# Kernel optimization log

Measured on AMD Instinct MI355X. Metric: run time of the kernel, lower is better.

## Reference

```python
import jax, jax.numpy as jnp
import numpy as np

ALPHA = 0.2  # LeakyReLU negative slope
EPS = 1e-8


def setup_inputs() -> dict:
    key = jax.random.key(0)
    k1, k2, k3, k4, k5 = jax.random.split(key, 5)
    N, D = 8192, 64  # square bipartite graph (required by the module's broadcasting)
    return {
        "user_embeddings": jax.random.normal(k1, (N, D), dtype=jnp.float32),
        "item_embeddings": jax.random.normal(k2, (N, D), dtype=jnp.float32),
        "adjacency_matrix": jax.random.uniform(k3, (N, N), dtype=jnp.float32),
        "W1": jax.random.normal(k4, (D, D), dtype=jnp.float32),
        "W2": jax.random.normal(k5, (D, D), dtype=jnp.float32),
    }


def _propagate(src, tgt, adj_st, W1, W2):
    """Fused NGCF message passing.

    Naive math: msg[a, b, :] = (src @ W1)[b, :] + (src[a] * tgt[b]) @ W2
                agg[a, :]    = sum_b adj_st[a, b] * msg[a, b, :]
    The sum over b distributes, so we never build the [N, N, D] tensor:
      agg = adj_st @ (src @ W1) + (src * (adj_st @ tgt)) @ W2
    """
    agg = adj_st @ (src @ W1) + (src * (adj_st @ tgt)) @ W2
    return jax.nn.leaky_relu(agg + tgt, negative_slope=ALPHA)


def reference(user_embeddings, item_embeddings, adjacency_matrix, W1, W2):
    # symmetric (sqrt of row-degree * col-degree) normalization
    row_sum = adjacency_matrix.sum(axis=1, keepdims=True)  # [N_u, 1]
    col_sum = adjacency_matrix.sum(axis=0, keepdims=True)  # [1, N_i]
    A = adjacency_matrix / (jnp.sqrt(row_sum * col_sum) + EPS)

    # item -> user messages use A^T; user -> item messages use A
    updated_user = _propagate(item_embeddings, user_embeddings, A.T, W1, W2)
    updated_item = _propagate(user_embeddings, item_embeddings, A, W1, W2)
    return (updated_user, updated_item)
```

## Files before the change

### kernel.cpp

```cpp
#include <hip/hip_runtime.h>
#include <hip/hip_bf16.h>


#define LRELU_ALPHA 0.2f
constexpr int N = 8192;
constexpr int KSPLIT = 8;
constexpr int KC = N / KSPLIT;

typedef __attribute__((ext_vector_type(4))) float f32x4;
typedef __attribute__((ext_vector_type(8))) __bf16 bf16x8;

__device__ __forceinline__ unsigned short f2bf(float x) {
    unsigned u = __builtin_bit_cast(unsigned, x);
    u += 0x7fffu + ((u >> 16) & 1u);
    return (unsigned short)(u >> 16);
}
__device__ __forceinline__ f32x4 mfma16(uint4 a, uint4 b, f32x4 c) {
    return __builtin_amdgcn_mfma_f32_16x16x32_bf16(
        __builtin_bit_cast(bf16x8, a), __builtin_bit_cast(bf16x8, b), c, 0, 0, 0);
}
__device__ __forceinline__ void stage16(const void* g, void* l) {
    __builtin_amdgcn_global_load_lds(
        (const __attribute__((address_space(1))) unsigned int*)g,
        (__attribute__((address_space(3))) unsigned int*)l, 16, 0, 0);
}

__global__ __launch_bounds__(256) void pass1_kernel(
    const float* __restrict__ adj,
    float* __restrict__ rs, float* __restrict__ cs,
    unsigned short* __restrict__ adjbf, unsigned short* __restrict__ adjT) {
    __shared__ unsigned short tile[128 * 128];
    __shared__ float rowsumL[128];
    __shared__ float4 colpart4[8][32];
    const int tid = threadIdx.x;
    const int g32 = tid >> 5, l32 = tid & 31;
    const int r0 = blockIdx.y * 128, c0 = blockIdx.x * 128;

    float4 colacc = make_float4(0.f, 0.f, 0.f, 0.f);
#pragma unroll 4
    for (int s = 0; s < 16; ++s) {
        const int i = s * 8 + g32;
        float4 v = *reinterpret_cast<const float4*>(adj + (size_t)(r0 + i) * N + c0 + l32 * 4);
        colacc.x += v.x; colacc.y += v.y; colacc.z += v.z; colacc.w += v.w;
        ushort4 b;
        b.x = f2bf(v.x); b.y = f2bf(v.y); b.z = f2bf(v.z); b.w = f2bf(v.w);
        *reinterpret_cast<ushort4*>(adjbf + (size_t)(r0 + i) * N + c0 + l32 * 4) = b;
        const int csw = l32 ^ (i & 31);
        *reinterpret_cast<ushort4*>(&tile[i * 128 + csw * 4]) = b;
        float rp = (v.x + v.y) + (v.z + v.w);
#pragma unroll
        for (int off = 16; off > 0; off >>= 1) rp += __shfl_down(rp, off, 32);
        if (l32 == 0) rowsumL[i] = rp;
    }
    colpart4[g32][l32] = colacc;
    __syncthreads();

    if (tid < 128) {
        atomicAdd(rs + r0 + tid, rowsumL[tid]);
        const float* cp = (const float*)colpart4;
        float s = 0.f;
#pragma unroll
        for (int w = 0; w < 8; ++w) s += cp[w * 128 + tid];
        atomicAdd(cs + c0 + tid, s);
    }

    const int i_loc = tid & 127;
    const int jhalf = tid >> 7;
#pragma unroll 8
    for (int jj = 0; jj < 64; ++jj) {
        const int j = jhalf * 64 + jj;
        unsigned short v = tile[i_loc * 128 + (((j >> 2) ^ (i_loc & 31)) * 4) + (j & 3)];
        adjT[(size_t)(c0 + j) * N + r0 + i_loc] = v;
    }
}

__global__ __launch_bounds__(256) void prep_kernel(
    const float* __restrict__ user, const float* __restrict__ item,
    const float* __restrict__ W1, const float* __restrict__ rs, const float* __restrict__ cs,
    unsigned short* __restrict__ Bti, unsigned short* __restrict__ Btu) {
    __shared__ float W1s[64][65];
    __shared__ float ru[64][65];
    __shared__ float ri[64][65];
    __shared__ unsigned short tile[128][66];
    const int tid = threadIdx.x;
    const int j0 = blockIdx.x * 64;
    for (int t = tid; t < 64 * 64; t += 256) {
        W1s[t >> 6][t & 63] = W1[t];
        ru[t >> 6][t & 63] = user[(size_t)j0 * 64 + t];
        ri[t >> 6][t & 63] = item[(size_t)j0 * 64 + t];
    }
    __syncthreads();
    for (int pass = 0; pass < 2; ++pass) {
        for (int it = 0; it < 32; ++it) {
            int idx = tid + 256 * it;
            int d = idx & 127, jl = idx >> 7;
            float scale = (pass == 0) ? rsqrtf(cs[j0 + jl]) : rsqrtf(rs[j0 + jl]);
            float v;
            if (d < 64) {
                const float(*src)[65] = (pass == 0) ? ru : ri;
                float acc = 0.f;
#pragma unroll
                for (int k = 0; k < 64; ++k) acc += src[jl][k] * W1s[k][d];
                v = acc;
            } else {
                const float(*src)[65] = (pass == 0) ? ri : ru;
                v = src[jl][d - 64];
            }
            tile[d][jl] = f2bf(v * scale);
        }
        __syncthreads();
        unsigned short* Bt = (pass == 0) ? Bti : Btu;
        for (int t = tid; t < 128 * 64; t += 256) {
            int d = t >> 6, jl = t & 63;
            Bt[(size_t)d * N + j0 + jl] = tile[d][jl];
        }
        __syncthreads();
    }
}

__global__ __launch_bounds__(256, 3) void gemm_kernel(
    const unsigned short* __restrict__ A0, const unsigned short* __restrict__ A1,
    const unsigned short* __restrict__ B0, const unsigned short* __restrict__ B1,
    float* __restrict__ P0, float* __restrict__ P1) {
    __shared__ unsigned short As[128 * 64];
    __shared__ unsigned short Bs[128 * 64];
    const unsigned short* __restrict__ A = blockIdx.z ? A1 : A0;
    const unsigned short* __restrict__ Bt = blockIdx.z ? B1 : B0;
    float* __restrict__ P = blockIdx.z ? P1 : P0;

    const int lane = threadIdx.x & 63, wave = threadIdx.x >> 6;
    const int q = lane >> 4, lm = lane & 15;
    const int wr = wave >> 1, wc = wave & 1;
    const int m0 = blockIdx.x * 128;
    const int kbase = blockIdx.y * KC;

    const int sr = wave * 32 + (lane >> 3);
    const int sc = lane & 7;

    f32x4 acc[4][4];
#pragma unroll
    for (int mt = 0; mt < 4; ++mt)
#pragma unroll
        for (int nt = 0; nt < 4; ++nt) acc[mt][nt] = (f32x4){0.f, 0.f, 0.f, 0.f};

    for (int step = 0; step < KC / 64; ++step) {
        const int k0 = kbase + step * 64;
#pragma unroll
        for (int t = 0; t < 4; ++t) {
            const int r = sr + t * 8;
            const int koff = (sc ^ (r & 7)) * 8;
            stage16(A + (size_t)(m0 + r) * N + k0 + koff, &As[(wave * 32 + t * 8) * 64]);
            stage16(Bt + (size_t)r * N + k0 + koff, &Bs[(wave * 32 + t * 8) * 64]);
        }
        __syncthreads();
#pragma unroll
        for (int kk = 0; kk < 2; ++kk) {
            uint4 af[4], bf[4];
#pragma unroll
            for (int mt = 0; mt < 4; ++mt) {
                const int ml = wr * 64 + mt * 16 + lm;
                af[mt] = *reinterpret_cast<const uint4*>(
                    &As[ml * 64 + (((kk * 4 + q) ^ (ml & 7)) * 8)]);
            }
#pragma unroll
            for (int nt = 0; nt < 4; ++nt) {
                const int nl = wc * 64 + nt * 16 + lm;
                bf[nt] = *reinterpret_cast<const uint4*>(
                    &Bs[nl * 64 + (((kk * 4 + q) ^ (nl & 7)) * 8)]);
            }
#pragma unroll
            for (int mt = 0; mt < 4; ++mt)
#pragma unroll
                for (int nt = 0; nt < 4; ++nt)
                    acc[mt][nt] = mfma16(af[mt], bf[nt], acc[mt][nt]);
        }
        __syncthreads();
    }

#pragma unroll
    for (int mt = 0; mt < 4; ++mt)
#pragma unroll
        for (int nt = 0; nt < 4; ++nt)
#pragma unroll
            for (int r = 0; r < 4; ++r) {
                const int row = m0 + wr * 64 + mt * 16 + q * 4 + r;
                const int col = wc * 64 + nt * 16 + lm;
                atomicAdd(&P[(size_t)row * 128 + col], acc[mt][nt][r]);
            }
}

__global__ __launch_bounds__(256) void epilogue_kernel(
    const float* __restrict__ user, const float* __restrict__ item,
    const float* __restrict__ W2, const float* __restrict__ rs, const float* __restrict__ cs,
    const float* __restrict__ Pi, const float* __restrict__ Pu,
    float* __restrict__ out) {
    __shared__ float W2s[64][65];
    __shared__ float gi[4][64];
    __shared__ float gu[4][64];
    const int tid = threadIdx.x;
    for (int t = tid; t < 64 * 64; t += 256) W2s[t >> 6][t & 63] = W2[t];
    const int r4 = tid >> 6, d = tid & 63;
    for (int p = 0; p < 4; ++p) {
        const int row = blockIdx.x * 16 + p * 4 + r4;
        const float invr = rsqrtf(rs[row]);
        const float invc = rsqrtf(cs[row]);
        const float u_rd = user[(size_t)row * 64 + d];
        const float i_rd = item[(size_t)row * 64 + d];
        __syncthreads();
        gi[r4][d] = u_rd * invr * Pi[(size_t)row * 128 + 64 + d];
        gu[r4][d] = i_rd * invc * Pu[(size_t)row * 128 + 64 + d];
        __syncthreads();
        float vi = invr * Pi[(size_t)row * 128 + d] + i_rd;
        float vu = invc * Pu[(size_t)row * 128 + d] + u_rd;
#pragma unroll
        for (int e = 0; e < 64; ++e) {
            vi += gi[r4][e] * W2s[e][d];
            vu += gu[r4][e] * W2s[e][d];
        }
        vi = vi > 0.f ? vi : LRELU_ALPHA * vi;
        vu = vu > 0.f ? vu : LRELU_ALPHA * vu;
        out[(size_t)row * 64 + d] = vu;
        out[(size_t)N * 64 + (size_t)row * 64 + d] = vi;
    }
}

extern "C" void kernel_launch(void* const* d_in, const int* in_sizes, int n_in,
                              void* d_out, int out_size, void* d_ws, size_t ws_size,
                              hipStream_t stream) {
    const float* user = (const float*)d_in[0];
    const float* item = (const float*)d_in[1];
    const float* adj  = (const float*)d_in[2];
    const float* W1   = (const float*)d_in[3];
    const float* W2   = (const float*)d_in[4];
    float* out = (float*)d_out;

    char* w = (char*)d_ws;
    float* Pi = (float*)w;  w += (size_t)N * 128 * 4;
    float* Pu = (float*)w;  w += (size_t)N * 128 * 4;
    float* rs = (float*)w;  w += (size_t)N * 4;
    float* cs = (float*)w;  w += (size_t)N * 4;
    unsigned short* Bti = (unsigned short*)w;  w += (size_t)N * 128 * 2;
    unsigned short* Btu = (unsigned short*)w;  w += (size_t)N * 128 * 2;
    unsigned short* adjbf = (unsigned short*)w;  w += (size_t)N * N * 2;
    unsigned short* adjT  = (unsigned short*)w;

    (void)hipMemsetAsync(Pi, 0, ((size_t)2 * N * 128 + 2 * N) * 4, stream);

    pass1_kernel<<<dim3(N / 128, N / 128), 256, 0, stream>>>(adj, rs, cs, adjbf, adjT);
    prep_kernel<<<N / 64, 256, 0, stream>>>(user, item, W1, rs, cs, Bti, Btu);
    gemm_kernel<<<dim3(N / 128, KSPLIT, 2), 256, 0, stream>>>(adjbf, adjT, Bti, Btu, Pi, Pu);
    epilogue_kernel<<<N / 16, 256, 0, stream>>>(user, item, W2, rs, cs, Pi, Pu, out);
}
```

Before: 558.9 us.

## Drop materialized transposed adjacency; transpose tiles in LDS inside a dedicated GEMM

Pass1 no longer writes a transposed bf16 copy of the adjacency matrix, which saves a 128 MB write and the matching read. A new gemmT kernel reads the row-major bf16 adjacency with plain vector loads and transposes each tile into LDS with an XOR swizzle before the MFMAs. The single batched GEMM launch becomes two launches. The transposed path does scalar 2-byte LDS stores and has no async staging for A, so its inner loop may be slower.

```diff
diff --git a/kernel.cpp b/kernel.cpp
--- a/kernel.cpp
+++ b/kernel.cpp
@@ -28,8 +28,7 @@
 __global__ __launch_bounds__(256) void pass1_kernel(
     const float* __restrict__ adj,
     float* __restrict__ rs, float* __restrict__ cs,
-    unsigned short* __restrict__ adjbf, unsigned short* __restrict__ adjT) {
-    __shared__ unsigned short tile[128 * 128];
+    unsigned short* __restrict__ adjbf) {
     __shared__ float rowsumL[128];
     __shared__ float4 colpart4[8][32];
     const int tid = threadIdx.x;
@@ -45,8 +44,6 @@
         ushort4 b;
         b.x = f2bf(v.x); b.y = f2bf(v.y); b.z = f2bf(v.z); b.w = f2bf(v.w);
         *reinterpret_cast<ushort4*>(adjbf + (size_t)(r0 + i) * N + c0 + l32 * 4) = b;
-        const int csw = l32 ^ (i & 31);
-        *reinterpret_cast<ushort4*>(&tile[i * 128 + csw * 4]) = b;
         float rp = (v.x + v.y) + (v.z + v.w);
 #pragma unroll
         for (int off = 16; off > 0; off >>= 1) rp += __shfl_down(rp, off, 32);
@@ -62,15 +59,6 @@
 #pragma unroll
         for (int w = 0; w < 8; ++w) s += cp[w * 128 + tid];
         atomicAdd(cs + c0 + tid, s);
-    }
-
-    const int i_loc = tid & 127;
-    const int jhalf = tid >> 7;
-#pragma unroll 8
-    for (int jj = 0; jj < 64; ++jj) {
-        const int j = jhalf * 64 + jj;
-        unsigned short v = tile[i_loc * 128 + (((j >> 2) ^ (i_loc & 31)) * 4) + (j & 3)];
-        adjT[(size_t)(c0 + j) * N + r0 + i_loc] = v;
     }
 }
 
@@ -118,15 +106,11 @@
     }
 }
 
-__global__ __launch_bounds__(256, 3) void gemm_kernel(
-    const unsigned short* __restrict__ A0, const unsigned short* __restrict__ A1,
-    const unsigned short* __restrict__ B0, const unsigned short* __restrict__ B1,
-    float* __restrict__ P0, float* __restrict__ P1) {
+__global__ __launch_bounds__(256, 3) void gemmN_kernel(
+    const unsigned short* __restrict__ A, const unsigned short* __restrict__ Bt,
+    float* __restrict__ P) {
     __shared__ unsigned short As[128 * 64];
     __shared__ unsigned short Bs[128 * 64];
-    const unsigned short* __restrict__ A = blockIdx.z ? A1 : A0;
-    const unsigned short* __restrict__ Bt = blockIdx.z ? B1 : B0;
-    float* __restrict__ P = blockIdx.z ? P1 : P0;
 
     const int lane = threadIdx.x & 63, wave = threadIdx.x >> 6;
     const int q = lane >> 4, lm = lane & 15;
@@ -184,6 +168,88 @@
 #pragma unroll
             for (int r = 0; r < 4; ++r) {
                 const int row = m0 + wr * 64 + mt * 16 + q * 4 + r;
+                const int col = wc * 64 + nt * 16 + lm;
+                atomicAdd(&P[(size_t)row * 128 + col], acc[mt][nt][r]);
+            }
+}
+
+__global__ __launch_bounds__(256, 3) void gemmT_kernel(
+    const unsigned short* __restrict__ A, const unsigned short* __restrict__ Bt,
+    float* __restrict__ P) {
+    __shared__ unsigned short Ts[128 * 64];
+    __shared__ unsigned short Bs[128 * 64];
+
+    const int lane = threadIdx.x & 63, wave = threadIdx.x >> 6;
+    const int q = lane >> 4, lm = lane & 15;
+    const int wr = wave >> 1, wc = wave & 1;
+    const int j0 = blockIdx.x * 128;
+    const int kbase = blockIdx.y * KC;
+
+    const int sr = wave * 32 + (lane >> 3);
+    const int sc = lane & 7;
+
+    f32x4 acc[4][4];
+#pragma unroll
+    for (int mt = 0; mt < 4; ++mt)
+#pragma unroll
+        for (int nt = 0; nt < 4; ++nt) acc[mt][nt] = (f32x4){0.f, 0.f, 0.f, 0.f};
+
+    for (int step = 0; step < KC / 64; ++step) {
+        const int ibase = kbase + step * 64;
+        uint4 g[4];
+#pragma unroll
+        for (int p = 0; p < 4; ++p) {
+            const int jc = wave + p * 4;
+            g[p] = *reinterpret_cast<const uint4*>(
+                A + (size_t)(ibase + lane) * N + j0 + jc * 8);
+        }
+        __syncthreads();
+#pragma unroll
+        for (int t = 0; t < 4; ++t) {
+            const int r = sr + t * 8;
+            const int koff = (sc ^ (r & 7)) * 8;
+            stage16(Bt + (size_t)r * N + ibase + koff, &Bs[(wave * 32 + t * 8) * 64]);
+        }
+#pragma unroll
+        for (int p = 0; p < 4; ++p) {
+            const int jl = (wave + p * 4) * 8;
+            const unsigned short* e = reinterpret_cast<const unsigned short*>(&g[p]);
+#pragma unroll
+            for (int k = 0; k < 8; ++k) {
+                Ts[(jl + k) * 64 + (lane ^ (k * 8))] = e[k];
+            }
+        }
+        __syncthreads();
+#pragma unroll
+        for (int kk = 0; kk < 2; ++kk) {
+            uint4 af[4], bf[4];
+#pragma unroll
+            for (int mt = 0; mt < 4; ++mt) {
+                const int ml = wr * 64 + mt * 16 + lm;
+                af[mt] = *reinterpret_cast<const uint4*>(
+                    &Ts[ml * 64 + ((kk * 32 + q * 8) ^ ((ml & 7) * 8))]);
+            }
+#pragma unroll
+            for (int nt = 0; nt < 4; ++nt) {
+                const int nl = wc * 64 + nt * 16 + lm;
+                bf[nt] = *reinterpret_cast<const uint4*>(
+                    &Bs[nl * 64 + (((kk * 4 + q) ^ (nl & 7)) * 8)]);
+            }
+#pragma unroll
+            for (int mt = 0; mt < 4; ++mt)
+#pragma unroll
+                for (int nt = 0; nt < 4; ++nt)
+                    acc[mt][nt] = mfma16(af[mt], bf[nt], acc[mt][nt]);
+        }
+    }
+
+#pragma unroll
+    for (int mt = 0; mt < 4; ++mt)
+#pragma unroll
+        for (int nt = 0; nt < 4; ++nt)
+#pragma unroll
+            for (int r = 0; r < 4; ++r) {
+                const int row = j0 + wr * 64 + mt * 16 + q * 4 + r;
                 const int col = wc * 64 + nt * 16 + lm;
                 atomicAdd(&P[(size_t)row * 128 + col], acc[mt][nt][r]);
             }
@@ -241,13 +307,13 @@
     float* cs = (float*)w;  w += (size_t)N * 4;
     unsigned short* Bti = (unsigned short*)w;  w += (size_t)N * 128 * 2;
     unsigned short* Btu = (unsigned short*)w;  w += (size_t)N * 128 * 2;
-    unsigned short* adjbf = (unsigned short*)w;  w += (size_t)N * N * 2;
-    unsigned short* adjT  = (unsigned short*)w;
+    unsigned short* adjbf = (unsigned short*)w;
 
     (void)hipMemsetAsync(Pi, 0, ((size_t)2 * N * 128 + 2 * N) * 4, stream);
 
-    pass1_kernel<<<dim3(N / 128, N / 128), 256, 0, stream>>>(adj, rs, cs, adjbf, adjT);
+    pass1_kernel<<<dim3(N / 128, N / 128), 256, 0, stream>>>(adj, rs, cs, adjbf);
     prep_kernel<<<N / 64, 256, 0, stream>>>(user, item, W1, rs, cs, Bti, Btu);
-    gemm_kernel<<<dim3(N / 128, KSPLIT, 2), 256, 0, stream>>>(adjbf, adjT, Bti, Btu, Pi, Pu);
+    gemmN_kernel<<<dim3(N / 128, KSPLIT), 256, 0, stream>>>(adjbf, Bti, Pi);
+    gemmT_kernel<<<dim3(N / 128, KSPLIT), 256, 0, stream>>>(adjbf, Btu, Pu);
     epilogue_kernel<<<N / 16, 256, 0, stream>>>(user, item, W2, rs, cs, Pi, Pu, out);
 }
```

Result: faster. 538.3 us (-3.7%).
